# Kernel optimization log

Hardware: AMD Instinct MI355X
Metric: run time of the kernel (lower is better)

Reference implementation:

```python
import jax, jax.numpy as jnp
import numpy as np

UNITS = 1024

def setup_inputs() -> dict:
    key = jax.random.key(0)
    k1, k2, k3 = jax.random.split(key, 3)
    B, T, F = 128, 256, 4
    sequence = jax.random.normal(k1, (B, T, F), dtype=jnp.float32)
    # small init scale keeps the ReLU cell state from exploding over 256 steps
    W = jax.random.normal(k2, (F, 4 * UNITS), dtype=jnp.float32) * 0.05
    U = jax.random.normal(k3, (UNITS, 4 * UNITS), dtype=jnp.float32) * 0.02
    b = jnp.zeros((4 * UNITS,), dtype=jnp.float32)
    return {"sequence": sequence, "W": W, "U": U, "b": b}

def _lstm_relu(sequence, W, U, b):
    B = sequence.shape[0]
    h0 = jnp.zeros((B, UNITS), dtype=sequence.dtype)
    c0 = jnp.zeros((B, UNITS), dtype=sequence.dtype)
    # precompute input projections for all timesteps: [T, B, 4H]
    x_proj = jnp.einsum('btf,fg->tbg', sequence, W) + b

    def step(carry, xp_t):
        h, c = carry
        z = xp_t + h @ U  # [B, 4H], gate order i,f,c,o (Keras)
        zi, zf, zg, zo = jnp.split(z, 4, axis=-1)
        i = jax.nn.sigmoid(zi)
        f = jax.nn.sigmoid(zf)
        g = jax.nn.relu(zg)          # activation=relu for candidate
        o = jax.nn.sigmoid(zo)
        c_new = f * c + i * g
        h_new = o * jax.nn.relu(c_new)  # activation=relu on cell output
        return (h_new, c_new), h_new

    (h_last, c_last), outs = jax.lax.scan(step, (h0, c0), x_proj)
    output = jnp.transpose(outs, (1, 0, 2))  # [B, T, H]
    return output, h_last, c_last

def reference(sequence, W, U, b):
    return _lstm_relu(sequence, W, U, b)
```

## Files before the change

kernel.cpp:

```cpp
#include <hip/hip_runtime.h>
#include <hip/hip_bf16.h>
#include <cstdint>


#define B_SZ   128
#define T_SZ   256
#define H_SZ   1024
#define G_SZ   4096
#define ULD    130

typedef __attribute__((ext_vector_type(8))) short short8;
typedef __attribute__((ext_vector_type(4))) float f32x4;
typedef __attribute__((ext_vector_type(2))) float f32x2;

__device__ __forceinline__ short f2bf(float f) {
    union { float f; unsigned u; } a; a.f = f;
    unsigned r = a.u + 0x7fffu + ((a.u >> 16) & 1u);
    return (short)(r >> 16);
}

__device__ __forceinline__ float sigmoidf_(float x) {
    return 1.0f / (1.0f + __expf(-x));
}

__device__ __forceinline__ short8 pack8(f32x4 a, f32x4 b) {
    union { f32x4 v; unsigned u[4]; } ua, ub; ua.v = a; ub.v = b;
    union { short8 s; unsigned d[4]; } r;
    r.d[0] = __builtin_amdgcn_perm(ua.u[1] + 0x8000u, ua.u[0] + 0x8000u, 0x07060302u);
    r.d[1] = __builtin_amdgcn_perm(ua.u[3] + 0x8000u, ua.u[2] + 0x8000u, 0x07060302u);
    r.d[2] = __builtin_amdgcn_perm(ub.u[1] + 0x8000u, ub.u[0] + 0x8000u, 0x07060302u);
    r.d[3] = __builtin_amdgcn_perm(ub.u[3] + 0x8000u, ub.u[2] + 0x8000u, 0x07060302u);
    return r.s;
}

template<int BF16EX>
__global__ __launch_bounds__(256, 1)
void lstm_persistent(const float* __restrict__ x, const float* __restrict__ W,
                     const float* __restrict__ U, const float* __restrict__ bias,
                     float* __restrict__ out, unsigned* __restrict__ flags,
                     short* __restrict__ ex)
{
    __shared__ __align__(16) char smem[66560];
    short* Ust   = (short*)smem;
    float* zpA   = (float*)smem;
    float* zpB   = (float*)(smem + 32768);

    const int tid  = threadIdx.x;
    const int bid  = blockIdx.x;
    const int rb   = bid >> 6;
    const int jb   = bid & 63;
    const int w    = tid >> 6;
    const int lane = tid & 63;
    const int q    = lane >> 4;
    const int n    = lane & 15;

    short8 bfrag[8][4];
    for (int kc = 0; kc < 4; ++kc) {
        const int kbase = kc * 256;
        for (int i = tid; i < 256 * 64; i += 256) {
            int k = i >> 6, col = i & 63;
            int gcol = (col >> 4) * 1024 + jb * 16 + (col & 15);
            Ust[k * ULD + col] = f2bf(U[(size_t)(kbase + k) * G_SZ + gcol]);
        }
        __syncthreads();
        if (w == kc) {
            #pragma unroll
            for (int kk = 0; kk < 8; ++kk) {
                #pragma unroll
                for (int g = 0; g < 4; ++g) {
                    short8 bb;
                    #pragma unroll
                    for (int jj = 0; jj < 8; ++jj)
                        bb[jj] = Ust[(kk * 32 + q * 8 + jj) * ULD + g * 16 + n];
                    bfrag[kk][g] = bb;
                }
            }
        }
        __syncthreads();
    }

    const int row_l  = tid >> 4;
    const int hid_l  = tid & 15;
    const int hid_g  = jb * 16 + hid_l;
    const int row_g0 = rb * 32 + row_l;
    const int row_g1 = row_g0 + 16;
    const int qr = row_l >> 2, vr = row_l & 3;
    float Wr[4][4], br[4];
    #pragma unroll
    for (int g = 0; g < 4; ++g) {
        br[g] = bias[g * 1024 + hid_g];
        #pragma unroll
        for (int f = 0; f < 4; ++f)
            Wr[g][f] = W[(size_t)f * G_SZ + g * 1024 + hid_g];
    }
    float c0 = 0.f, c1 = 0.f;

    const int arow0 = tid >= 0 ? rb * 32 + n : 0;
    const int krow  = w * 256 + q * 8;
    const unsigned* pollp = flags + rb * 256 + w * 64 + lane;
    unsigned* pubp = flags + rb * 256 + jb * 4 + w;

    for (int t = 0; t < T_SZ; ++t) {
        f32x4 xv0 = *(const f32x4*)(x + ((size_t)row_g0 * T_SZ + t) * 4);
        f32x4 xv1 = *(const f32x4*)(x + ((size_t)row_g1 * T_SZ + t) * 4);

        short8 af[8][2];
        if (t == 0) {
            short8 z = {};
            #pragma unroll
            for (int kk = 0; kk < 8; ++kk) { af[kk][0] = z; af[kk][1] = z; }
        } else {
            for (;;) {
                unsigned v = __hip_atomic_load(pollp, __ATOMIC_RELAXED,
                                               __HIP_MEMORY_SCOPE_AGENT);
                if (__all((int)(v >= (unsigned)t))) break;
                __builtin_amdgcn_s_sleep(2);
            }
            __atomic_signal_fence(__ATOMIC_ACQUIRE);

            if (BF16EX) {
                #pragma unroll
                for (int kk = 0; kk < 8; ++kk) {
                    #pragma unroll
                    for (int mt = 0; mt < 2; ++mt) {
                        const short* p = ex +
                            ((size_t)(arow0 + mt * 16) * T_SZ + (t - 1)) * H_SZ +
                            krow + kk * 32;
                        af[kk][mt] = *(const short8*)p;
                    }
                }
            } else {
                #pragma unroll
                for (int kk = 0; kk < 8; ++kk) {
                    #pragma unroll
                    for (int mt = 0; mt < 2; ++mt) {
                        const float* p = out +
                            ((size_t)(arow0 + mt * 16) * T_SZ + (t - 1)) * H_SZ +
                            krow + kk * 32;
                        f32x4 lo = *(const f32x4*)p;
                        f32x4 hi = *(const f32x4*)(p + 4);
                        af[kk][mt] = pack8(lo, hi);
                    }
                }
            }
        }

        f32x4 acc[2][4];
        #pragma unroll
        for (int mt = 0; mt < 2; ++mt)
            #pragma unroll
            for (int g = 0; g < 4; ++g)
                acc[mt][g] = (f32x4){0.f, 0.f, 0.f, 0.f};

        #pragma unroll
        for (int kk = 0; kk < 8; ++kk)
            #pragma unroll
            for (int mt = 0; mt < 2; ++mt)
                #pragma unroll
                for (int g = 0; g < 4; ++g)
                    acc[mt][g] = __builtin_amdgcn_mfma_f32_16x16x32_bf16(
                        af[kk][mt], bfrag[kk][g], acc[mt][g], 0, 0, 0);

        float* zp = (t & 1) ? zpB : zpA;
        #pragma unroll
        for (int mt = 0; mt < 2; ++mt)
            #pragma unroll
            for (int g = 0; g < 4; ++g)
                *(f32x4*)&zp[(((w * 2 + mt) * 4 + g) * 4 + q) * 64 + n * 4] =
                    acc[mt][g];
        __syncthreads();

        float hn0, hn1;
        {
            float z[4];
            #pragma unroll
            for (int g = 0; g < 4; ++g) {
                float s = br[g];
                #pragma unroll
                for (int ww = 0; ww < 4; ++ww)
                    s += zp[(((ww * 2 + 0) * 4 + g) * 4 + qr) * 64 + hid_l * 4 + vr];
                s += xv0[0] * Wr[g][0] + xv0[1] * Wr[g][1] +
                     xv0[2] * Wr[g][2] + xv0[3] * Wr[g][3];
                z[g] = s;
            }
            float ig = sigmoidf_(z[0]), fg = sigmoidf_(z[1]);
            float gg = fmaxf(z[2], 0.f), og = sigmoidf_(z[3]);
            c0 = fg * c0 + ig * gg;
            hn0 = og * fmaxf(c0, 0.f);
        }
        {
            float z[4];
            #pragma unroll
            for (int g = 0; g < 4; ++g) {
                float s = br[g];
                #pragma unroll
                for (int ww = 0; ww < 4; ++ww)
                    s += zp[(((ww * 2 + 1) * 4 + g) * 4 + qr) * 64 + hid_l * 4 + vr];
                s += xv1[0] * Wr[g][0] + xv1[1] * Wr[g][1] +
                     xv1[2] * Wr[g][2] + xv1[3] * Wr[g][3];
                z[g] = s;
            }
            float ig = sigmoidf_(z[0]), fg = sigmoidf_(z[1]);
            float gg = fmaxf(z[2], 0.f), og = sigmoidf_(z[3]);
            c1 = fg * c1 + ig * gg;
            hn1 = og * fmaxf(c1, 0.f);
        }

        const size_t ob0 = ((size_t)row_g0 * T_SZ + t) * H_SZ + hid_g;
        const size_t ob1 = ((size_t)row_g1 * T_SZ + t) * H_SZ + hid_g;

        if (BF16EX) {
            float o0 = __shfl_down(hn0, 1);
            float o1 = __shfl_down(hn1, 1);
            if ((hid_l & 1) == 0) {
                unsigned w0 = (unsigned)(unsigned short)f2bf(hn0) |
                              ((unsigned)(unsigned short)f2bf(o0) << 16);
                unsigned w1 = (unsigned)(unsigned short)f2bf(hn1) |
                              ((unsigned)(unsigned short)f2bf(o1) << 16);
                __hip_atomic_store((unsigned*)&ex[ob0], w0, __ATOMIC_RELAXED,
                                   __HIP_MEMORY_SCOPE_AGENT);
                __hip_atomic_store((unsigned*)&ex[ob1], w1, __ATOMIC_RELAXED,
                                   __HIP_MEMORY_SCOPE_AGENT);
            }
            if (t != T_SZ - 1) {
                asm volatile("s_waitcnt vmcnt(0)" ::: "memory");
                if (lane == 0)
                    __hip_atomic_store(pubp, (unsigned)(t + 1),
                                       __ATOMIC_RELAXED, __HIP_MEMORY_SCOPE_AGENT);
            }
            out[ob0] = hn0;
            out[ob1] = hn1;
        } else {
            __hip_atomic_store((unsigned*)&out[ob0], __float_as_uint(hn0),
                               __ATOMIC_RELAXED, __HIP_MEMORY_SCOPE_AGENT);
            __hip_atomic_store((unsigned*)&out[ob1], __float_as_uint(hn1),
                               __ATOMIC_RELAXED, __HIP_MEMORY_SCOPE_AGENT);
            if (t != T_SZ - 1) {
                asm volatile("s_waitcnt vmcnt(0)" ::: "memory");
                if (lane == 0)
                    __hip_atomic_store(pubp, (unsigned)(t + 1),
                                       __ATOMIC_RELAXED, __HIP_MEMORY_SCOPE_AGENT);
            }
        }

        if (t == T_SZ - 1) {
            float* hlast = out + (size_t)B_SZ * T_SZ * H_SZ;
            float* clast = hlast + (size_t)B_SZ * H_SZ;
            hlast[(size_t)row_g0 * H_SZ + hid_g] = hn0;
            hlast[(size_t)row_g1 * H_SZ + hid_g] = hn1;
            clast[(size_t)row_g0 * H_SZ + hid_g] = c0;
            clast[(size_t)row_g1 * H_SZ + hid_g] = c1;
        }
    }
}

extern "C" void kernel_launch(void* const* d_in, const int* in_sizes, int n_in,
                              void* d_out, int out_size, void* d_ws, size_t ws_size,
                              hipStream_t stream) {
    const float* x    = (const float*)d_in[0];
    const float* W    = (const float*)d_in[1];
    const float* U    = (const float*)d_in[2];
    const float* bias = (const float*)d_in[3];
    float* out = (float*)d_out;

    unsigned* flags = (unsigned*)d_ws;
    short* ex = (short*)((char*)d_ws + 4096);

    hipMemsetAsync(d_ws, 0, 4096, stream);

    const size_t need = 4096 + (size_t)B_SZ * T_SZ * H_SZ * sizeof(short);
    if (ws_size >= need) {
        hipLaunchKernelGGL((lstm_persistent<1>), dim3(256), dim3(256), 0, stream,
                           x, W, U, bias, out, flags, ex);
    } else {
        hipLaunchKernelGGL((lstm_persistent<0>), dim3(256), dim3(256), 0, stream,
                           x, W, U, bias, out, flags, ex);
    }
}
```

Before: 1.668 ms.

## Use bf16 exchange data sign bits as readiness sentinel instead of flag polling

The bf16 hidden-state exchange buffer is pre-filled with 0x80 bytes, so every not-yet-written element is negative. Since h is always non-negative, consumers read the previous step's h directly and check the sign bits; only if a sentinel is still present do they fall back to polling flags and re-reading with atomic loads. This removes the separate store-flag, wait, load-flag round trip from the critical path of each timestep. In exchange it adds a memset of the whole exchange buffer on every launch and changes what the published flag means.

```diff
diff --git a/kernel.cpp b/kernel.cpp
--- a/kernel.cpp
+++ b/kernel.cpp
@@ -11,7 +11,6 @@
 
 typedef __attribute__((ext_vector_type(8))) short short8;
 typedef __attribute__((ext_vector_type(4))) float f32x4;
-typedef __attribute__((ext_vector_type(2))) float f32x2;
 
 __device__ __forceinline__ short f2bf(float f) {
     union { float f; unsigned u; } a; a.f = f;
@@ -28,6 +27,7 @@
     union { short8 s; unsigned d[4]; } r;
     r.d[0] = __builtin_amdgcn_perm(ua.u[1] + 0x8000u, ua.u[0] + 0x8000u, 0x07060302u);
     r.d[1] = __builtin_amdgcn_perm(ua.u[3] + 0x8000u, ua.u[2] + 0x8000u, 0x07060302u);
+    r.d[2] = __builtin_amdgcn_perm(ub.u[1] + 0x8000u, ub.u[2 - 2] + 0x8000u, 0x07060302u);
     r.d[2] = __builtin_amdgcn_perm(ub.u[1] + 0x8000u, ub.u[0] + 0x8000u, 0x07060302u);
     r.d[3] = __builtin_amdgcn_perm(ub.u[3] + 0x8000u, ub.u[2] + 0x8000u, 0x07060302u);
     return r.s;
@@ -95,7 +95,7 @@
     }
     float c0 = 0.f, c1 = 0.f;
 
-    const int arow0 = tid >= 0 ? rb * 32 + n : 0;
+    const int arow0 = rb * 32 + n;
     const int krow  = w * 256 + q * 8;
     const unsigned* pollp = flags + rb * 256 + w * 64 + lane;
     unsigned* pubp = flags + rb * 256 + jb * 4 + w;
@@ -109,6 +109,56 @@
             short8 z = {};
             #pragma unroll
             for (int kk = 0; kk < 8; ++kk) { af[kk][0] = z; af[kk][1] = z; }
+        } else if (BF16EX) {
+            #pragma unroll
+            for (int kk = 0; kk < 8; ++kk)
+                #pragma unroll
+                for (int mt = 0; mt < 2; ++mt)
+                    af[kk][mt] = *(const short8*)(ex +
+                        ((size_t)(arow0 + mt * 16) * T_SZ + (t - 1)) * H_SZ +
+                        krow + kk * 32);
+            asm volatile("s_waitcnt vmcnt(0)" ::: "memory");
+            if (lane == 0)
+                __hip_atomic_store(pubp, (unsigned)t, __ATOMIC_RELAXED,
+                                   __HIP_MEMORY_SCOPE_AGENT);
+            unsigned orv = 0u;
+            #pragma unroll
+            for (int kk = 0; kk < 8; ++kk)
+                #pragma unroll
+                for (int mt = 0; mt < 2; ++mt) {
+                    union { short8 s; unsigned u[4]; } cv; cv.s = af[kk][mt];
+                    orv |= cv.u[0] | cv.u[1] | cv.u[2] | cv.u[3];
+                }
+            if (!__all((int)((orv & 0x80008000u) == 0u))) {
+                for (;;) {
+                    unsigned v = __hip_atomic_load(pollp, __ATOMIC_RELAXED,
+                                                   __HIP_MEMORY_SCOPE_AGENT);
+                    if (__all((int)(v >= (unsigned)t))) break;
+                    __builtin_amdgcn_s_sleep(2);
+                }
+                __atomic_signal_fence(__ATOMIC_ACQUIRE);
+                for (;;) {
+                    unsigned orv2 = 0u;
+                    #pragma unroll
+                    for (int kk = 0; kk < 8; ++kk)
+                        #pragma unroll
+                        for (int mt = 0; mt < 2; ++mt) {
+                            const unsigned* pu = (const unsigned*)(ex +
+                                ((size_t)(arow0 + mt * 16) * T_SZ + (t - 1)) * H_SZ +
+                                krow + kk * 32);
+                            union { short8 s; unsigned u[4]; } cv;
+                            #pragma unroll
+                            for (int d = 0; d < 4; ++d) {
+                                cv.u[d] = __hip_atomic_load(pu + d, __ATOMIC_RELAXED,
+                                                            __HIP_MEMORY_SCOPE_AGENT);
+                                orv2 |= cv.u[d];
+                            }
+                            af[kk][mt] = cv.s;
+                        }
+                    if (__all((int)((orv2 & 0x80008000u) == 0u))) break;
+                    __builtin_amdgcn_s_sleep(2);
+                }
+            }
         } else {
             for (;;) {
                 unsigned v = __hip_atomic_load(pollp, __ATOMIC_RELAXED,
@@ -117,30 +167,16 @@
                 __builtin_amdgcn_s_sleep(2);
             }
             __atomic_signal_fence(__ATOMIC_ACQUIRE);
-
-            if (BF16EX) {
-                #pragma unroll
-                for (int kk = 0; kk < 8; ++kk) {
-                    #pragma unroll
-                    for (int mt = 0; mt < 2; ++mt) {
-                        const short* p = ex +
-                            ((size_t)(arow0 + mt * 16) * T_SZ + (t - 1)) * H_SZ +
-                            krow + kk * 32;
-                        af[kk][mt] = *(const short8*)p;
-                    }
-                }
-            } else {
-                #pragma unroll
-                for (int kk = 0; kk < 8; ++kk) {
-                    #pragma unroll
-                    for (int mt = 0; mt < 2; ++mt) {
-                        const float* p = out +
-                            ((size_t)(arow0 + mt * 16) * T_SZ + (t - 1)) * H_SZ +
-                            krow + kk * 32;
-                        f32x4 lo = *(const f32x4*)p;
-                        f32x4 hi = *(const f32x4*)(p + 4);
-                        af[kk][mt] = pack8(lo, hi);
-                    }
+            #pragma unroll
+            for (int kk = 0; kk < 8; ++kk) {
+                #pragma unroll
+                for (int mt = 0; mt < 2; ++mt) {
+                    const float* p = out +
+                        ((size_t)(arow0 + mt * 16) * T_SZ + (t - 1)) * H_SZ +
+                        krow + kk * 32;
+                    f32x4 lo = *(const f32x4*)p;
+                    f32x4 hi = *(const f32x4*)(p + 4);
+                    af[kk][mt] = pack8(lo, hi);
                 }
             }
         }
@@ -222,12 +258,6 @@
                 __hip_atomic_store((unsigned*)&ex[ob1], w1, __ATOMIC_RELAXED,
                                    __HIP_MEMORY_SCOPE_AGENT);
             }
-            if (t != T_SZ - 1) {
-                asm volatile("s_waitcnt vmcnt(0)" ::: "memory");
-                if (lane == 0)
-                    __hip_atomic_store(pubp, (unsigned)(t + 1),
-                                       __ATOMIC_RELAXED, __HIP_MEMORY_SCOPE_AGENT);
-            }
             out[ob0] = hn0;
             out[ob1] = hn1;
         } else {
@@ -266,10 +296,13 @@
     unsigned* flags = (unsigned*)d_ws;
     short* ex = (short*)((char*)d_ws + 4096);
 
+    const size_t exbytes = (size_t)B_SZ * T_SZ * H_SZ * sizeof(short);
+    const size_t need = 4096 + exbytes;
+
     hipMemsetAsync(d_ws, 0, 4096, stream);
 
-    const size_t need = 4096 + (size_t)B_SZ * T_SZ * H_SZ * sizeof(short);
     if (ws_size >= need) {
+        hipMemsetAsync(ex, 0x80, exbytes, stream);
         hipLaunchKernelGGL((lstm_persistent<1>), dim3(256), dim3(256), 0, stream,
                            x, W, U, bias, out, flags, ex);
     } else {
```

Result: slower. 3.830 ms (+129.6%).

## Split per-step handoff into two half-tile flags to overlap compute and publish

Applied to the files above, without the earlier changes.

Each block now publishes its hidden-state output in two halves (rows 0-15 and 16-31), each with its own flag array. Consumers wait on the first flag, load that half and run its MFMAs while the second half is still being produced. The input projection is also hoisted ahead of the polling wait. The aim is to shorten the critical path of the cross-block step dependency, at the cost of extra flag traffic and a second polling loop.

```diff
diff --git a/kernel.cpp b/kernel.cpp
--- a/kernel.cpp
+++ b/kernel.cpp
@@ -11,7 +11,6 @@
 
 typedef __attribute__((ext_vector_type(8))) short short8;
 typedef __attribute__((ext_vector_type(4))) float f32x4;
-typedef __attribute__((ext_vector_type(2))) float f32x2;
 
 __device__ __forceinline__ short f2bf(float f) {
     union { float f; unsigned u; } a; a.f = f;
@@ -37,8 +36,8 @@
 __global__ __launch_bounds__(256, 1)
 void lstm_persistent(const float* __restrict__ x, const float* __restrict__ W,
                      const float* __restrict__ U, const float* __restrict__ bias,
-                     float* __restrict__ out, unsigned* __restrict__ flags,
-                     short* __restrict__ ex)
+                     float* __restrict__ out, unsigned* __restrict__ flagsA,
+                     unsigned* __restrict__ flagsB, short* __restrict__ ex)
 {
     __shared__ __align__(16) char smem[66560];
     short* Ust   = (short*)smem;
@@ -95,52 +94,72 @@
     }
     float c0 = 0.f, c1 = 0.f;
 
-    const int arow0 = tid >= 0 ? rb * 32 + n : 0;
+    const int arow0 = rb * 32 + n;
     const int krow  = w * 256 + q * 8;
-    const unsigned* pollp = flags + rb * 256 + w * 64 + lane;
-    unsigned* pubp = flags + rb * 256 + jb * 4 + w;
+    const unsigned* pollpA = flagsA + rb * 256 + w * 64 + lane;
+    const unsigned* pollpB = flagsB + rb * 256 + w * 64 + lane;
+    unsigned* pubpA = flagsA + rb * 256 + jb * 4 + w;
+    unsigned* pubpB = flagsB + rb * 256 + jb * 4 + w;
 
     for (int t = 0; t < T_SZ; ++t) {
         f32x4 xv0 = *(const f32x4*)(x + ((size_t)row_g0 * T_SZ + t) * 4);
         f32x4 xv1 = *(const f32x4*)(x + ((size_t)row_g1 * T_SZ + t) * 4);
+        float zb0[4], zb1[4];
+        #pragma unroll
+        for (int g = 0; g < 4; ++g) {
+            zb0[g] = br[g] + xv0[0] * Wr[g][0] + xv0[1] * Wr[g][1] +
+                     xv0[2] * Wr[g][2] + xv0[3] * Wr[g][3];
+            zb1[g] = br[g] + xv1[0] * Wr[g][0] + xv1[1] * Wr[g][1] +
+                     xv1[2] * Wr[g][2] + xv1[3] * Wr[g][3];
+        }
 
         short8 af[8][2];
         if (t == 0) {
             short8 z = {};
             #pragma unroll
             for (int kk = 0; kk < 8; ++kk) { af[kk][0] = z; af[kk][1] = z; }
-        } else {
+        } else if (BF16EX) {
             for (;;) {
-                unsigned v = __hip_atomic_load(pollp, __ATOMIC_RELAXED,
+                unsigned v = __hip_atomic_load(pollpA, __ATOMIC_RELAXED,
                                                __HIP_MEMORY_SCOPE_AGENT);
                 if (__all((int)(v >= (unsigned)t))) break;
                 __builtin_amdgcn_s_sleep(2);
             }
             __atomic_signal_fence(__ATOMIC_ACQUIRE);
-
-            if (BF16EX) {
+            #pragma unroll
+            for (int kk = 0; kk < 8; ++kk)
+                af[kk][0] = *(const short8*)(ex +
+                    ((size_t)arow0 * T_SZ + (t - 1)) * H_SZ + krow + kk * 32);
+            asm volatile("" ::: "memory");
+            for (;;) {
+                unsigned v = __hip_atomic_load(pollpB, __ATOMIC_RELAXED,
+                                               __HIP_MEMORY_SCOPE_AGENT);
+                if (__all((int)(v >= (unsigned)t))) break;
+                __builtin_amdgcn_s_sleep(2);
+            }
+            __atomic_signal_fence(__ATOMIC_ACQUIRE);
+            #pragma unroll
+            for (int kk = 0; kk < 8; ++kk)
+                af[kk][1] = *(const short8*)(ex +
+                    ((size_t)(arow0 + 16) * T_SZ + (t - 1)) * H_SZ + krow + kk * 32);
+        } else {
+            for (;;) {
+                unsigned v = __hip_atomic_load(pollpA, __ATOMIC_RELAXED,
+                                               __HIP_MEMORY_SCOPE_AGENT);
+                if (__all((int)(v >= (unsigned)t))) break;
+                __builtin_amdgcn_s_sleep(2);
+            }
+            __atomic_signal_fence(__ATOMIC_ACQUIRE);
+            #pragma unroll
+            for (int kk = 0; kk < 8; ++kk) {
                 #pragma unroll
-                for (int kk = 0; kk < 8; ++kk) {
-                    #pragma unroll
-                    for (int mt = 0; mt < 2; ++mt) {
-                        const short* p = ex +
-                            ((size_t)(arow0 + mt * 16) * T_SZ + (t - 1)) * H_SZ +
-                            krow + kk * 32;
-                        af[kk][mt] = *(const short8*)p;
-                    }
-                }
-            } else {
-                #pragma unroll
-                for (int kk = 0; kk < 8; ++kk) {
-                    #pragma unroll
-                    for (int mt = 0; mt < 2; ++mt) {
-                        const float* p = out +
-                            ((size_t)(arow0 + mt * 16) * T_SZ + (t - 1)) * H_SZ +
-                            krow + kk * 32;
-                        f32x4 lo = *(const f32x4*)p;
-                        f32x4 hi = *(const f32x4*)(p + 4);
-                        af[kk][mt] = pack8(lo, hi);
-                    }
+                for (int mt = 0; mt < 2; ++mt) {
+                    const float* p = out +
+                        ((size_t)(arow0 + mt * 16) * T_SZ + (t - 1)) * H_SZ +
+                        krow + kk * 32;
+                    f32x4 lo = *(const f32x4*)p;
+                    f32x4 hi = *(const f32x4*)(p + 4);
+                    af[kk][mt] = pack8(lo, hi);
                 }
             }
         }
@@ -155,11 +174,15 @@
         #pragma unroll
         for (int kk = 0; kk < 8; ++kk)
             #pragma unroll
-            for (int mt = 0; mt < 2; ++mt)
-                #pragma unroll
-                for (int g = 0; g < 4; ++g)
-                    acc[mt][g] = __builtin_amdgcn_mfma_f32_16x16x32_bf16(
-                        af[kk][mt], bfrag[kk][g], acc[mt][g], 0, 0, 0);
+            for (int g = 0; g < 4; ++g)
+                acc[0][g] = __builtin_amdgcn_mfma_f32_16x16x32_bf16(
+                    af[kk][0], bfrag[kk][g], acc[0][g], 0, 0, 0);
+        #pragma unroll
+        for (int kk = 0; kk < 8; ++kk)
+            #pragma unroll
+            for (int g = 0; g < 4; ++g)
+                acc[1][g] = __builtin_amdgcn_mfma_f32_16x16x32_bf16(
+                    af[kk][1], bfrag[kk][g], acc[1][g], 0, 0, 0);
 
         float* zp = (t & 1) ? zpB : zpA;
         #pragma unroll
@@ -170,17 +193,18 @@
                     acc[mt][g];
         __syncthreads();
 
-        float hn0, hn1;
+        const size_t ob0 = ((size_t)row_g0 * T_SZ + t) * H_SZ + hid_g;
+        const size_t ob1 = ((size_t)row_g1 * T_SZ + t) * H_SZ + hid_g;
+
+        float hn0;
         {
             float z[4];
             #pragma unroll
             for (int g = 0; g < 4; ++g) {
-                float s = br[g];
+                float s = zb0[g];
                 #pragma unroll
                 for (int ww = 0; ww < 4; ++ww)
                     s += zp[(((ww * 2 + 0) * 4 + g) * 4 + qr) * 64 + hid_l * 4 + vr];
-                s += xv0[0] * Wr[g][0] + xv0[1] * Wr[g][1] +
-                     xv0[2] * Wr[g][2] + xv0[3] * Wr[g][3];
                 z[g] = s;
             }
             float ig = sigmoidf_(z[0]), fg = sigmoidf_(z[1]);
@@ -188,16 +212,25 @@
             c0 = fg * c0 + ig * gg;
             hn0 = og * fmaxf(c0, 0.f);
         }
+        if (BF16EX) {
+            float o0 = __shfl_down(hn0, 1);
+            if ((hid_l & 1) == 0) {
+                unsigned d0 = (unsigned)(unsigned short)f2bf(hn0) |
+                              ((unsigned)(unsigned short)f2bf(o0) << 16);
+                __hip_atomic_store((unsigned*)&ex[ob0], d0, __ATOMIC_RELAXED,
+                                   __HIP_MEMORY_SCOPE_AGENT);
+            }
+        }
+
+        float hn1;
         {
             float z[4];
             #pragma unroll
             for (int g = 0; g < 4; ++g) {
-                float s = br[g];
+                float s = zb1[g];
                 #pragma unroll
                 for (int ww = 0; ww < 4; ++ww)
                     s += zp[(((ww * 2 + 1) * 4 + g) * 4 + qr) * 64 + hid_l * 4 + vr];
-                s += xv1[0] * Wr[g][0] + xv1[1] * Wr[g][1] +
-                     xv1[2] * Wr[g][2] + xv1[3] * Wr[g][3];
                 z[g] = s;
             }
             float ig = sigmoidf_(z[0]), fg = sigmoidf_(z[1]);
@@ -206,26 +239,22 @@
             hn1 = og * fmaxf(c1, 0.f);
         }
 
-        const size_t ob0 = ((size_t)row_g0 * T_SZ + t) * H_SZ + hid_g;
-        const size_t ob1 = ((size_t)row_g1 * T_SZ + t) * H_SZ + hid_g;
-
         if (BF16EX) {
-            float o0 = __shfl_down(hn0, 1);
             float o1 = __shfl_down(hn1, 1);
             if ((hid_l & 1) == 0) {
-                unsigned w0 = (unsigned)(unsigned short)f2bf(hn0) |
-                              ((unsigned)(unsigned short)f2bf(o0) << 16);
-                unsigned w1 = (unsigned)(unsigned short)f2bf(hn1) |
+                unsigned d1 = (unsigned)(unsigned short)f2bf(hn1) |
                               ((unsigned)(unsigned short)f2bf(o1) << 16);
-                __hip_atomic_store((unsigned*)&ex[ob0], w0, __ATOMIC_RELAXED,
+                __hip_atomic_store((unsigned*)&ex[ob1], d1, __ATOMIC_RELAXED,
                                    __HIP_MEMORY_SCOPE_AGENT);
-                __hip_atomic_store((unsigned*)&ex[ob1], w1, __ATOMIC_RELAXED,
-                                   __HIP_MEMORY_SCOPE_AGENT);
             }
             if (t != T_SZ - 1) {
+                asm volatile("s_waitcnt vmcnt(1)" ::: "memory");
+                if (lane == 0)
+                    __hip_atomic_store(pubpA, (unsigned)(t + 1),
+                                       __ATOMIC_RELAXED, __HIP_MEMORY_SCOPE_AGENT);
                 asm volatile("s_waitcnt vmcnt(0)" ::: "memory");
                 if (lane == 0)
-                    __hip_atomic_store(pubp, (unsigned)(t + 1),
+                    __hip_atomic_store(pubpB, (unsigned)(t + 1),
                                        __ATOMIC_RELAXED, __HIP_MEMORY_SCOPE_AGENT);
             }
             out[ob0] = hn0;
@@ -238,7 +267,7 @@
             if (t != T_SZ - 1) {
                 asm volatile("s_waitcnt vmcnt(0)" ::: "memory");
                 if (lane == 0)
-                    __hip_atomic_store(pubp, (unsigned)(t + 1),
+                    __hip_atomic_store(pubpA, (unsigned)(t + 1),
                                        __ATOMIC_RELAXED, __HIP_MEMORY_SCOPE_AGENT);
             }
         }
@@ -263,17 +292,18 @@
     const float* bias = (const float*)d_in[3];
     float* out = (float*)d_out;
 
-    unsigned* flags = (unsigned*)d_ws;
-    short* ex = (short*)((char*)d_ws + 4096);
-
-    hipMemsetAsync(d_ws, 0, 4096, stream);
-
-    const size_t need = 4096 + (size_t)B_SZ * T_SZ * H_SZ * sizeof(short);
+    unsigned* flagsA = (unsigned*)d_ws;
+    unsigned* flagsB = (unsigned*)((char*)d_ws + 4096);
+    short* ex = (short*)((char*)d_ws + 8192);
+
+    hipMemsetAsync(d_ws, 0, 8192, stream);
+
+    const size_t need = 8192 + (size_t)B_SZ * T_SZ * H_SZ * sizeof(short);
     if (ws_size >= need) {
         hipLaunchKernelGGL((lstm_persistent<1>), dim3(256), dim3(256), 0, stream,
-                           x, W, U, bias, out, flags, ex);
+                           x, W, U, bias, out, flagsA, flagsB, ex);
     } else {
         hipLaunchKernelGGL((lstm_persistent<0>), dim3(256), dim3(256), 0, stream,
-                           x, W, U, bias, out, flags, ex);
+                           x, W, U, bias, out, flagsA, flagsB, ex);
     }
 }
```

Measured after the change: 1.413 ms. 15.3% less time.
